# Optimization experiments

Measured on AMD Instinct MI355X. Metric: run time of the kernel, lower is better.

The kernel has to match this reference:

```python
import jax, jax.numpy as jnp
import numpy as np

EPS = 1e-3  # matches torch module eps
NUM_FEATURES = 64


def setup_inputs() -> dict:
    key = jax.random.key(0)
    X = jax.random.normal(key, (128, NUM_FEATURES, 56, 56), dtype=jnp.float32)
    return {"X": X}


def reference(X):
    # Training-mode decorrelated batch norm (ZCA whitening via eigendecomposition).
    N, C = X.shape[0], X.shape[1]
    # [N, C, H, W] -> [C, N*H*W]
    x = jnp.reshape(jnp.swapaxes(X, 0, 1), (C, -1))
    m = x.shape[1]
    mean = jnp.mean(x, axis=-1, keepdims=True)
    xc = x - mean
    # sigma = eps*I + (1/m) * xc @ xc^T   (C x C, SPD)
    sigma = EPS * jnp.eye(C, dtype=X.dtype) + (xc @ xc.T) / m
    # SVD of an SPD matrix == eigendecomposition; use symmetric eigh.
    eig, u = jnp.linalg.eigh(sigma)
    # wm = u @ diag(eig^-1/2) @ u^T  (inverse matrix square root)
    wm = (u * jax.lax.rsqrt(eig)) @ u.T
    xn = wm @ xc  # whiten
    # [C, N*H*W] -> [N, C, H, W]
    Xn = jnp.swapaxes(jnp.reshape(xn, (C, N) + X.shape[2:]), 0, 1)
    return Xn
```

## Files before the change

### kernel.cpp

```cpp
#include <hip/hip_runtime.h>
#include <stdint.h>

#define CCH   64
#define HWSZ  3136
#define NB    128
#define MCOLS 401408
#define TK    128
#define NTILES 3136
#define LDK   136
#define LDB   72
#define SLOT  4160
#define WS_TAIL 16512
#define RG    32
#define K1MAX 1024
#define LDT   72

typedef short bf16x8 __attribute__((ext_vector_type(8)));
typedef float f32x4  __attribute__((ext_vector_type(4)));
typedef unsigned short u16x4 __attribute__((ext_vector_type(4)));

__device__ __forceinline__ unsigned short f2bf(float f) {
    union { float f; uint32_t u; } v; v.f = f;
    uint32_t r = v.u + 0x7fffu + ((v.u >> 16) & 1u);
    return (unsigned short)(r >> 16);
}
__device__ __forceinline__ float bf2f(unsigned short h) {
    union { uint32_t u; float f; } v; v.u = ((uint32_t)h) << 16; return v.f;
}

__global__ __launch_bounds__(256) void k1_gram(const float* __restrict__ X,
                                               float* __restrict__ part,
                                               int nb) {
    __shared__ __align__(16) unsigned short tile[CCH * LDK];
    const int tid = threadIdx.x;
    const int w = tid >> 6, l = tid & 63;

    f32x4 acc[4];
    #pragma unroll
    for (int b = 0; b < 4; ++b) acc[b] = (f32x4){0.f, 0.f, 0.f, 0.f};
    float sacc[16];
    #pragma unroll
    for (int i = 0; i < 16; ++i) sacc[i] = 0.f;

    float2 xv[16];

    uint32_t t = blockIdx.x;
    {
        const uint32_t s = t * TK + 2u * (uint32_t)l;
        const uint32_t n = s / HWSZ;
        const uint32_t hw = s - n * HWSZ;
        const size_t base = (size_t)n * (CCH * HWSZ) + hw + (size_t)w * HWSZ;
        #pragma unroll
        for (int i = 0; i < 16; ++i)
            xv[i] = *(const float2*)(X + base + (size_t)i * (4u * HWSZ));
    }

    for (;;) {
        __syncthreads();
        #pragma unroll
        for (int i = 0; i < 16; ++i) {
            sacc[i] += xv[i].x + xv[i].y;
            const int c = 4 * i + w;
            *(uint32_t*)&tile[c * LDK + 2 * l] =
                (uint32_t)f2bf(xv[i].x) | ((uint32_t)f2bf(xv[i].y) << 16);
        }
        __syncthreads();

        const uint32_t tn = t + (uint32_t)nb;
        const bool more = tn < NTILES;
        if (more) {
            const uint32_t s = tn * TK + 2u * (uint32_t)l;
            const uint32_t n = s / HWSZ;
            const uint32_t hw = s - n * HWSZ;
            const size_t base = (size_t)n * (CCH * HWSZ) + hw + (size_t)w * HWSZ;
            #pragma unroll
            for (int i = 0; i < 16; ++i)
                xv[i] = *(const float2*)(X + base + (size_t)i * (4u * HWSZ));
        }

        #pragma unroll
        for (int k0 = 0; k0 < TK; k0 += 32) {
            const int koff = k0 + ((l >> 4) << 3);
            const bf16x8 fa = *(const bf16x8*)&tile[(16 * w + (l & 15)) * LDK + koff];
            #pragma unroll
            for (int bj = 0; bj < 4; ++bj) {
                const bf16x8 fb = *(const bf16x8*)&tile[(16 * bj + (l & 15)) * LDK + koff];
                acc[bj] = __builtin_amdgcn_mfma_f32_16x16x32_bf16(fa, fb, acc[bj], 0, 0, 0);
            }
        }

        if (!more) break;
        t = tn;
    }

    float* pg = part + (size_t)blockIdx.x * SLOT;
    #pragma unroll
    for (int bj = 0; bj < 4; ++bj) {
        #pragma unroll
        for (int r = 0; r < 4; ++r) {
            const int row = 16 * w + ((l >> 4) << 2) + r;
            const int col = 16 * bj + (l & 15);
            pg[row * 64 + col] = acc[bj][r];
        }
    }
    #pragma unroll
    for (int i = 0; i < 16; ++i) {
        float v = sacc[i];
        #pragma unroll
        for (int m = 32; m > 0; m >>= 1) v += __shfl_xor(v, m, 64);
        if (l == 0) pg[4096 + 4 * i + w] = v;
    }
}

__global__ __launch_bounds__(256) void k1b1_reduce(const float* __restrict__ part,
                                                   float* __restrict__ part2,
                                                   int nb) {
    const int bx = blockIdx.x;
    const int g = bx / 17;
    const int e = (bx - g * 17) * 256 + threadIdx.x;
    if (e >= SLOT) return;
    float a0 = 0.f, a1 = 0.f, a2 = 0.f, a3 = 0.f;
    int b = g;
    for (; b + 3 * RG < nb; b += 4 * RG) {
        a0 += part[(size_t)b * SLOT + e];
        a1 += part[(size_t)(b + RG) * SLOT + e];
        a2 += part[(size_t)(b + 2 * RG) * SLOT + e];
        a3 += part[(size_t)(b + 3 * RG) * SLOT + e];
    }
    for (; b < nb; b += RG) a0 += part[(size_t)b * SLOT + e];
    part2[(size_t)g * SLOT + e] = (a0 + a1) + (a2 + a3);
}

__global__ __launch_bounds__(256) void k1b2_reduce(const float* __restrict__ part2,
                                                   float* __restrict__ out) {
    const int e = blockIdx.x * 256 + threadIdx.x;
    if (e >= SLOT) return;
    float a0 = 0.f, a1 = 0.f, a2 = 0.f, a3 = 0.f;
    #pragma unroll
    for (int b = 0; b < RG; b += 4) {
        a0 += part2[(size_t)b * SLOT + e];
        a1 += part2[(size_t)(b + 1) * SLOT + e];
        a2 += part2[(size_t)(b + 2) * SLOT + e];
        a3 += part2[(size_t)(b + 3) * SLOT + e];
    }
    out[e] = (a0 + a1) + (a2 + a3);
}

__device__ __forceinline__ bf16x8 ldfrag_h(const unsigned short* H, int rowbase, int k0, int l) {
    const int row = rowbase + (l & 15);
    const int koff = k0 + ((l >> 4) << 3);
    return *(const bf16x8*)&H[row * LDB + koff];
}
__device__ __forceinline__ bf16x8 ldfrag_lo(const float* F, bf16x8 hi, int rowbase, int k0, int l) {
    const int row = rowbase + (l & 15);
    const int koff = k0 + ((l >> 4) << 3);
    const float* p = F + row * 64 + koff;
    bf16x8 lo;
    #pragma unroll
    for (int j = 0; j < 8; ++j)
        lo[j] = (short)f2bf(p[j] - bf2f((unsigned short)hi[j]));
    return lo;
}

__device__ void mm_plain(const unsigned short* Lh, const unsigned short* Rh,
                         unsigned short* DH, float* DF, int tid) {
    const int w = tid >> 6, l = tid & 63;
    f32x4 acc[4];
    #pragma unroll
    for (int b = 0; b < 4; ++b) acc[b] = (f32x4){0.f, 0.f, 0.f, 0.f};
    #pragma unroll
    for (int k0 = 0; k0 < 64; k0 += 32) {
        const bf16x8 la = ldfrag_h(Lh, 16 * w, k0, l);
        #pragma unroll
        for (int b = 0; b < 4; ++b) {
            const bf16x8 rb = ldfrag_h(Rh, 16 * b, k0, l);
            acc[b] = __builtin_amdgcn_mfma_f32_16x16x32_bf16(la, rb, acc[b], 0, 0, 0);
        }
    }
    __syncthreads();
    #pragma unroll
    for (int b = 0; b < 4; ++b) {
        #pragma unroll
        for (int r = 0; r < 4; ++r) {
            const int row = 16 * w + ((l >> 4) << 2) + r;
            const int col = 16 * b + (l & 15);
            const float v = acc[b][r];
            if (DH) DH[row * LDB + col] = f2bf(v);
            if (DF) DF[row * 64 + col] = v;
        }
    }
    __syncthreads();
}

__device__ void mm_split(const unsigned short* Lh, const float* Lf,
                         const unsigned short* Rh, const float* Rf,
                         unsigned short* DH, float* DF, int tid) {
    const int w = tid >> 6, l = tid & 63;
    f32x4 acc[4];
    #pragma unroll
    for (int b = 0; b < 4; ++b) acc[b] = (f32x4){0.f, 0.f, 0.f, 0.f};
    #pragma unroll
    for (int k0 = 0; k0 < 64; k0 += 32) {
        const bf16x8 lah = ldfrag_h(Lh, 16 * w, k0, l);
        const bf16x8 lal = ldfrag_lo(Lf, lah, 16 * w, k0, l);
        #pragma unroll
        for (int b = 0; b < 4; ++b) {
            const bf16x8 rbh = ldfrag_h(Rh, 16 * b, k0, l);
            const bf16x8 rbl = ldfrag_lo(Rf, rbh, 16 * b, k0, l);
            acc[b] = __builtin_amdgcn_mfma_f32_16x16x32_bf16(lah, rbh, acc[b], 0, 0, 0);
            acc[b] = __builtin_amdgcn_mfma_f32_16x16x32_bf16(lah, rbl, acc[b], 0, 0, 0);
            acc[b] = __builtin_amdgcn_mfma_f32_16x16x32_bf16(lal, rbh, acc[b], 0, 0, 0);
        }
    }
    __syncthreads();
    #pragma unroll
    for (int b = 0; b < 4; ++b) {
        #pragma unroll
        for (int r = 0; r < 4; ++r) {
            const int row = 16 * w + ((l >> 4) << 2) + r;
            const int col = 16 * b + (l & 15);
            const float v = acc[b][r];
            if (DH) DH[row * LDB + col] = f2bf(v);
            if (DF) DF[row * 64 + col] = v;
        }
    }
    __syncthreads();
}

__global__ __launch_bounds__(256) void k2_ns(float* __restrict__ ws) {
    const float* gram = ws;
    const float* sums = ws + 4096;
    float* bvec = ws + 8256;
    float* Ag = ws + 8320;
    unsigned short* wmh = (unsigned short*)(ws + 12416);
    unsigned short* wml = (unsigned short*)(ws + 14464);

    __shared__ float Zf[4096];
    __shared__ float Sf[4096];
    __shared__ __align__(16) unsigned short Ah[64 * LDB];
    __shared__ __align__(16) unsigned short ZhA[64 * LDB];
    __shared__ __align__(16) unsigned short Bh[64 * LDB];
    __shared__ float mu[64];
    __shared__ float sred[1];

    const int tid = threadIdx.x;
    const float invm = 1.0f / (float)MCOLS;

    if (tid < 64) mu[tid] = sums[tid] * invm;
    __syncthreads();

    #pragma unroll
    for (int j = 0; j < 16; ++j) {
        const int e = tid * 16 + j;
        const int i = e >> 6, c = e & 63;
        Sf[e] = gram[e] * invm - mu[i] * mu[c] + ((i == c) ? 1e-3f : 0.0f);
    }
    __syncthreads();

    if (tid < 64) {
        float rs = 0.f;
        #pragma unroll
        for (int j = 0; j < 64; ++j) {
            const int c = (j + tid) & 63;
            rs += fabsf(Sf[tid * 64 + c]);
        }
        #pragma unroll
        for (int m = 32; m > 0; m >>= 1) rs = fmaxf(rs, __shfl_xor(rs, m, 64));
        if (tid == 0) sred[0] = rs;
    }
    __syncthreads();
    const float s = sred[0];
    const float invs = 1.0f / s;

    #pragma unroll
    for (int j = 0; j < 16; ++j) {
        const int e = tid * 16 + j;
        const int i = e >> 6, c = e & 63;
        const float a = Sf[e] * invs;
        Ag[e] = a;
        Ah[i * LDB + c] = f2bf(a);
        const float z = (i == c) ? 1.0f : 0.0f;
        Zf[e] = z;
        ZhA[i * LDB + c] = f2bf(z);
    }
    __syncthreads();

    for (int itn = 0; itn < 4; ++itn) {
        mm_plain(ZhA, ZhA, Bh, nullptr, tid);
        mm_plain(Ah, Bh, Bh, nullptr, tid);
        mm_plain(ZhA, Bh, nullptr, Sf, tid);
        #pragma unroll
        for (int j = 0; j < 16; ++j) {
            const int e = tid * 16 + j;
            const int i = e >> 6, c = e & 63;
            const float z = 1.5f * Zf[e] - 0.5f * Sf[e];
            Zf[e] = z;
            ZhA[i * LDB + c] = f2bf(z);
        }
        __syncthreads();
    }

    mm_split(ZhA, Zf, ZhA, Zf, Bh, Sf, tid);
    mm_split(Ah, Ag, Bh, Sf, Bh, Sf, tid);
    mm_split(ZhA, Zf, Bh, Sf, nullptr, Sf, tid);

    const float wsq = 1.0f / sqrtf(s);
    #pragma unroll
    for (int j = 0; j < 16; ++j) {
        const int e = tid * 16 + j;
        const float z = 1.5f * Zf[e] - 0.5f * Sf[e];
        Zf[e] = z;
        const float wv = z * wsq;
        const unsigned short h = f2bf(wv);
        wmh[e] = h;
        wml[e] = f2bf(wv - bf2f(h));
    }
    __syncthreads();

    if (tid < 64) {
        float acc = 0.f;
        #pragma unroll
        for (int j = 0; j < 64; ++j) {
            const int c = (j + tid) & 63;
            acc += Zf[tid * 64 + c] * mu[c];
        }
        bvec[tid] = acc * wsq;
    }
}

__global__ __launch_bounds__(256, 2) void k3_whiten(const float* __restrict__ X,
                                                    const float* __restrict__ ws,
                                                    float* __restrict__ out) {
    __shared__ __align__(16) unsigned short xh[64 * LDT];
    __shared__ __align__(16) unsigned short xl[64 * LDT];
    const int tid = threadIdx.x;
    const int w = tid >> 6, l = tid & 63;

    const unsigned short* __restrict__ wmh = (const unsigned short*)(ws + 12416);
    const unsigned short* __restrict__ wml = (const unsigned short*)(ws + 14464);
    const float* __restrict__ bvec = ws + 8256;

    const uint32_t g = blockIdx.x;
    const uint32_t n = g / 49u;
    const uint32_t hw0 = (g - n * 49u) * 64u;
    const size_t base = (size_t)n * (CCH * HWSZ) + hw0;

    #pragma unroll
    for (int u = 0; u < 4; ++u) {
        const int c0 = (w * 4 + u) * 4;
        float x0 = X[base + (size_t)(c0 + 0) * HWSZ + l];
        float x1 = X[base + (size_t)(c0 + 1) * HWSZ + l];
        float x2 = X[base + (size_t)(c0 + 2) * HWSZ + l];
        float x3 = X[base + (size_t)(c0 + 3) * HWSZ + l];
        u16x4 hv, lv;
        hv[0] = f2bf(x0); lv[0] = f2bf(x0 - bf2f(hv[0]));
        hv[1] = f2bf(x1); lv[1] = f2bf(x1 - bf2f(hv[1]));
        hv[2] = f2bf(x2); lv[2] = f2bf(x2 - bf2f(hv[2]));
        hv[3] = f2bf(x3); lv[3] = f2bf(x3 - bf2f(hv[3]));
        *(u16x4*)&xh[l * LDT + c0] = hv;
        *(u16x4*)&xl[l * LDT + c0] = lv;
    }
    __syncthreads();

    f32x4 acc[4];
    #pragma unroll
    for (int b = 0; b < 4; ++b) acc[b] = (f32x4){0.f, 0.f, 0.f, 0.f};

    const int frow = (16 * w + (l & 15)) * LDT;
    const int koffL = (l >> 4) << 3;
    #pragma unroll
    for (int k0 = 0; k0 < 64; k0 += 32) {
        const bf16x8 fah = *(const bf16x8*)&xh[frow + k0 + koffL];
        const bf16x8 fal = *(const bf16x8*)&xl[frow + k0 + koffL];
        #pragma unroll
        for (int cb = 0; cb < 4; ++cb) {
            const int c = cb * 16 + (l & 15);
            const bf16x8 fbh = *(const bf16x8*)&wmh[c * 64 + k0 + koffL];
            const bf16x8 fbl = *(const bf16x8*)&wml[c * 64 + k0 + koffL];
            acc[cb] = __builtin_amdgcn_mfma_f32_16x16x32_bf16(fah, fbh, acc[cb], 0, 0, 0);
            acc[cb] = __builtin_amdgcn_mfma_f32_16x16x32_bf16(fah, fbl, acc[cb], 0, 0, 0);
            acc[cb] = __builtin_amdgcn_mfma_f32_16x16x32_bf16(fal, fbh, acc[cb], 0, 0, 0);
        }
    }

    const int p0 = 16 * w + ((l >> 4) << 2);
    #pragma unroll
    for (int cb = 0; cb < 4; ++cb) {
        const int c = cb * 16 + (l & 15);
        const float bv = bvec[c];
        f32x4 v;
        v[0] = acc[cb][0] - bv;
        v[1] = acc[cb][1] - bv;
        v[2] = acc[cb][2] - bv;
        v[3] = acc[cb][3] - bv;
        *(f32x4*)&out[base + (size_t)c * HWSZ + p0] = v;
    }
}

extern "C" void kernel_launch(void* const* d_in, const int* in_sizes, int n_in,
                              void* d_out, int out_size, void* d_ws, size_t ws_size,
                              hipStream_t stream) {
    (void)in_sizes; (void)n_in; (void)out_size;
    const float* X = (const float*)d_in[0];
    float* out = (float*)d_out;
    float* ws = (float*)d_ws;

    long avail = (long)(ws_size / sizeof(float)) - WS_TAIL - (long)RG * SLOT;
    int nb = (int)(avail / SLOT);
    if (nb > K1MAX) nb = K1MAX;
    if (nb < 1) nb = 1;

    float* part = ws + WS_TAIL;
    float* part2 = part + (size_t)nb * SLOT;

    k1_gram<<<nb, 256, 0, stream>>>(X, part, nb);
    k1b1_reduce<<<17 * RG, 256, 0, stream>>>(part, part2, nb);
    k1b2_reduce<<<17, 256, 0, stream>>>(part2, ws);
    k2_ns<<<1, 256, 0, stream>>>(ws);
    k3_whiten<<<MCOLS / 64, 256, 0, stream>>>(X, ws, out);
}
```

Before: 269.5 us.

## Make whiten kernel persistent with register prefetch of next tile

The whiten kernel now launches a fixed grid of 1024 blocks instead of one block per 64-column tile, and each block loops over tiles in a grid-stride pattern. The whitening matrix fragments and bias are loaded into registers once per block. The next tile's inputs are prefetched into registers while the current tile's MFMAs and stores run. This is meant to hide global load latency and cut repeated per-block setup, at the cost of higher register pressure and dropping the 2-blocks-per-CU occupancy hint.

```diff
diff --git a/kernel.cpp b/kernel.cpp
--- a/kernel.cpp
+++ b/kernel.cpp
@@ -14,6 +14,8 @@
 #define RG    32
 #define K1MAX 1024
 #define LDT   72
+#define K3NB  1024
+#define K3T   6272
 
 typedef short bf16x8 __attribute__((ext_vector_type(8)));
 typedef float f32x4  __attribute__((ext_vector_type(4)));
@@ -328,72 +330,108 @@
     }
 }
 
-__global__ __launch_bounds__(256, 2) void k3_whiten(const float* __restrict__ X,
-                                                    const float* __restrict__ ws,
-                                                    float* __restrict__ out) {
+__global__ __launch_bounds__(256) void k3_whiten(const float* __restrict__ X,
+                                                 const float* __restrict__ ws,
+                                                 float* __restrict__ out) {
     __shared__ __align__(16) unsigned short xh[64 * LDT];
     __shared__ __align__(16) unsigned short xl[64 * LDT];
     const int tid = threadIdx.x;
     const int w = tid >> 6, l = tid & 63;
+    const int lm = l & 15;
+    const int koffL = (l >> 4) << 3;
 
     const unsigned short* __restrict__ wmh = (const unsigned short*)(ws + 12416);
     const unsigned short* __restrict__ wml = (const unsigned short*)(ws + 14464);
     const float* __restrict__ bvec = ws + 8256;
 
-    const uint32_t g = blockIdx.x;
-    const uint32_t n = g / 49u;
-    const uint32_t hw0 = (g - n * 49u) * 64u;
-    const size_t base = (size_t)n * (CCH * HWSZ) + hw0;
-
-    #pragma unroll
-    for (int u = 0; u < 4; ++u) {
-        const int c0 = (w * 4 + u) * 4;
-        float x0 = X[base + (size_t)(c0 + 0) * HWSZ + l];
-        float x1 = X[base + (size_t)(c0 + 1) * HWSZ + l];
-        float x2 = X[base + (size_t)(c0 + 2) * HWSZ + l];
-        float x3 = X[base + (size_t)(c0 + 3) * HWSZ + l];
-        u16x4 hv, lv;
-        hv[0] = f2bf(x0); lv[0] = f2bf(x0 - bf2f(hv[0]));
-        hv[1] = f2bf(x1); lv[1] = f2bf(x1 - bf2f(hv[1]));
-        hv[2] = f2bf(x2); lv[2] = f2bf(x2 - bf2f(hv[2]));
-        hv[3] = f2bf(x3); lv[3] = f2bf(x3 - bf2f(hv[3]));
-        *(u16x4*)&xh[l * LDT + c0] = hv;
-        *(u16x4*)&xl[l * LDT + c0] = lv;
-    }
-    __syncthreads();
-
-    f32x4 acc[4];
-    #pragma unroll
-    for (int b = 0; b < 4; ++b) acc[b] = (f32x4){0.f, 0.f, 0.f, 0.f};
-
-    const int frow = (16 * w + (l & 15)) * LDT;
-    const int koffL = (l >> 4) << 3;
-    #pragma unroll
-    for (int k0 = 0; k0 < 64; k0 += 32) {
-        const bf16x8 fah = *(const bf16x8*)&xh[frow + k0 + koffL];
-        const bf16x8 fal = *(const bf16x8*)&xl[frow + k0 + koffL];
+    bf16x8 fbh[2][4], fbl[2][4];
+    #pragma unroll
+    for (int kk = 0; kk < 2; ++kk) {
         #pragma unroll
         for (int cb = 0; cb < 4; ++cb) {
-            const int c = cb * 16 + (l & 15);
-            const bf16x8 fbh = *(const bf16x8*)&wmh[c * 64 + k0 + koffL];
-            const bf16x8 fbl = *(const bf16x8*)&wml[c * 64 + k0 + koffL];
-            acc[cb] = __builtin_amdgcn_mfma_f32_16x16x32_bf16(fah, fbh, acc[cb], 0, 0, 0);
-            acc[cb] = __builtin_amdgcn_mfma_f32_16x16x32_bf16(fah, fbl, acc[cb], 0, 0, 0);
-            acc[cb] = __builtin_amdgcn_mfma_f32_16x16x32_bf16(fal, fbh, acc[cb], 0, 0, 0);
-        }
-    }
-
+            const int c = cb * 16 + lm;
+            fbh[kk][cb] = *(const bf16x8*)&wmh[c * 64 + kk * 32 + koffL];
+            fbl[kk][cb] = *(const bf16x8*)&wml[c * 64 + kk * 32 + koffL];
+        }
+    }
+    float bv[4];
+    #pragma unroll
+    for (int cb = 0; cb < 4; ++cb) bv[cb] = bvec[cb * 16 + lm];
+
+    float xv[16];
+    uint32_t g = blockIdx.x;
+    size_t base;
+    {
+        const uint32_t n = g / 49u;
+        const uint32_t hw0 = (g - n * 49u) * 64u;
+        base = (size_t)n * (CCH * HWSZ) + hw0;
+        #pragma unroll
+        for (int u = 0; u < 16; ++u)
+            xv[u] = X[base + (size_t)(w * 16 + u) * HWSZ + l];
+    }
+
+    const int frow = (16 * w + lm) * LDT;
     const int p0 = 16 * w + ((l >> 4) << 2);
-    #pragma unroll
-    for (int cb = 0; cb < 4; ++cb) {
-        const int c = cb * 16 + (l & 15);
-        const float bv = bvec[c];
-        f32x4 v;
-        v[0] = acc[cb][0] - bv;
-        v[1] = acc[cb][1] - bv;
-        v[2] = acc[cb][2] - bv;
-        v[3] = acc[cb][3] - bv;
-        *(f32x4*)&out[base + (size_t)c * HWSZ + p0] = v;
+
+    for (;;) {
+        __syncthreads();
+        #pragma unroll
+        for (int uu = 0; uu < 4; ++uu) {
+            u16x4 hv, lv;
+            #pragma unroll
+            for (int j = 0; j < 4; ++j) {
+                const float x = xv[uu * 4 + j];
+                const unsigned short h = f2bf(x);
+                hv[j] = h;
+                lv[j] = f2bf(x - bf2f(h));
+            }
+            const int c0 = w * 16 + uu * 4;
+            *(u16x4*)&xh[l * LDT + c0] = hv;
+            *(u16x4*)&xl[l * LDT + c0] = lv;
+        }
+        __syncthreads();
+
+        const uint32_t gn = g + K3NB;
+        const bool more = gn < K3T;
+        size_t basen = 0;
+        if (more) {
+            const uint32_t n = gn / 49u;
+            const uint32_t hw0 = (gn - n * 49u) * 64u;
+            basen = (size_t)n * (CCH * HWSZ) + hw0;
+            #pragma unroll
+            for (int u = 0; u < 16; ++u)
+                xv[u] = X[basen + (size_t)(w * 16 + u) * HWSZ + l];
+        }
+
+        f32x4 acc[4];
+        #pragma unroll
+        for (int b = 0; b < 4; ++b) acc[b] = (f32x4){0.f, 0.f, 0.f, 0.f};
+        #pragma unroll
+        for (int kk = 0; kk < 2; ++kk) {
+            const bf16x8 fah = *(const bf16x8*)&xh[frow + kk * 32 + koffL];
+            const bf16x8 fal = *(const bf16x8*)&xl[frow + kk * 32 + koffL];
+            #pragma unroll
+            for (int cb = 0; cb < 4; ++cb) {
+                acc[cb] = __builtin_amdgcn_mfma_f32_16x16x32_bf16(fah, fbh[kk][cb], acc[cb], 0, 0, 0);
+                acc[cb] = __builtin_amdgcn_mfma_f32_16x16x32_bf16(fah, fbl[kk][cb], acc[cb], 0, 0, 0);
+                acc[cb] = __builtin_amdgcn_mfma_f32_16x16x32_bf16(fal, fbh[kk][cb], acc[cb], 0, 0, 0);
+            }
+        }
+
+        #pragma unroll
+        for (int cb = 0; cb < 4; ++cb) {
+            const int c = cb * 16 + lm;
+            f32x4 v;
+            v[0] = acc[cb][0] - bv[cb];
+            v[1] = acc[cb][1] - bv[cb];
+            v[2] = acc[cb][2] - bv[cb];
+            v[3] = acc[cb][3] - bv[cb];
+            *(f32x4*)&out[base + (size_t)c * HWSZ + p0] = v;
+        }
+
+        if (!more) break;
+        g = gn;
+        base = basen;
     }
 }
 
@@ -417,5 +455,5 @@
     k1b1_reduce<<<17 * RG, 256, 0, stream>>>(part, part2, nb);
     k1b2_reduce<<<17, 256, 0, stream>>>(part2, ws);
     k2_ns<<<1, 256, 0, stream>>>(ws);
-    k3_whiten<<<MCOLS / 64, 256, 0, stream>>>(X, ws, out);
-}
+    k3_whiten<<<K3NB, 256, 0, stream>>>(X, ws, out);
+}
```

Measured after the change: 242.8 us. -9.9%, faster.
